# Optimization experiments

Measured on AMD Instinct MI355X. Metric: run time of the kernel, lower is better.

Reference implementation:

```python
import jax, jax.numpy as jnp
import numpy as np

L = 26        # layers (hard-coded NUM_LAYERS)
B, T = 1, 16  # batch, query length
D = 768       # d_model
NH, NG = 8, 2 # heads, query groups
G = NH // NG  # group size
HD = 128      # head_dim
FF = 3072     # ffn hidden
V = 32000     # vocab
SC = 4096     # kv cache length
SOFTCAP = 50.0
EPS = 1e-6


def rms_norm(x, w):
    # zero-centered RMSNorm: x * rsqrt(mean(x^2)+eps) * (1 + w)
    ms = jnp.mean(jnp.square(x), axis=-1, keepdims=True)
    return x * jax.lax.rsqrt(ms + EPS) * (1.0 + w)


def apply_rope(x, cos, sin):
    d = x.shape[-1]
    xl, xr = x[..., : d // 2], x[..., d // 2 :]
    rot = jnp.concatenate([-xr, xl], axis=-1)
    return x * cos + rot * sin


def setup_inputs() -> dict:
    key = jax.random.key(0)
    ks = iter(jax.random.split(key, 40))
    n = lambda shape, s=1.0: jax.random.normal(next(ks), shape, jnp.float32) * s
    u = lambda shape: jax.random.uniform(next(ks), shape, jnp.float32)
    return {
        "embeddings": n((B, T, D)),
        "mask_global": jnp.zeros((B, 1, T, SC + T), jnp.float32),
        "mask_local": jnp.zeros((B, 1, T, SC + T), jnp.float32),
        "pos_emb_cos": u((1, T, 1, HD)),
        "pos_emb_sin": u((1, T, 1, HD)),
        "pos_emb_local_cos": u((1, T, 1, HD)),
        "pos_emb_local_sin": u((1, T, 1, HD)),
        "kv_cache_k": n((L, B, NG, SC, HD)),        # concat on axis 2 (seq)
        "kv_cache_v": n((L, B, NG, HD, SC)),        # concat on axis 3 (seq), V stored transposed
        "pre_attn_norm_w": n((L, D), 0.02),
        "qkv_w": n((L, NG * (G + 2) * HD, D), 0.02),
        "q_norm_w": n((L, HD), 0.02),
        "k_norm_w": n((L, HD), 0.02),
        "out_w": n((L, D, NH * HD), 0.02),
        "post_attn_norm_w": n((L, D), 0.02),
        "pre_ff_norm_w": n((L, D), 0.02),
        "gate_w": n((L, FF, D), 0.02),
        "up_w": n((L, FF, D), 0.02),
        "down_w": n((L, D, FF), 0.02),
        "post_ff_norm_w": n((L, D), 0.02),
        "final_norm_w": n((D,), 0.02),
        "lm_head_w": n((V, D), 0.02),
    }


def reference(embeddings, mask_global, mask_local, pos_emb_cos, pos_emb_sin,
              pos_emb_local_cos, pos_emb_local_sin, kv_cache_k, kv_cache_v,
              pre_attn_norm_w, qkv_w, q_norm_w, k_norm_w, out_w, post_attn_norm_w,
              pre_ff_norm_w, gate_w, up_w, down_w, post_ff_norm_w,
              final_norm_w, lm_head_w):
    is_local = jnp.array([(i + 1) % 6 == 0 for i in range(L)])
    scale = 1.0 / np.sqrt(HD)

    def layer(h, xs):
        pan, qkvw, qnw, knw, ow, postw, pfn, gw, uw, dw, pofn, kc, vc, loc = xs
        cos = jnp.where(loc, pos_emb_local_cos, pos_emb_cos)
        sin = jnp.where(loc, pos_emb_local_sin, pos_emb_sin)
        mask = jnp.where(loc, mask_local, mask_global)

        x = rms_norm(h, pan)
        qkv = jnp.einsum('btd,od->bto', x, qkvw)
        qkv = qkv.reshape(B, T, NG, G + 2, HD).transpose(0, 2, 1, 3, 4)  # [B,NG,T,G+2,HD]
        # faithful to torch: [B,NG,T,G,HD].reshape(B,NH,T,HD) (row-major), then -> [B,T,NH,HD]
        q = qkv[:, :, :, :G, :].reshape(B, NH, T, HD).transpose(0, 2, 1, 3)
        k = qkv[:, :, :, G, :].transpose(0, 2, 1, 3)      # [B,T,NG,HD]
        v = qkv[:, :, :, G + 1, :].transpose(0, 2, 1, 3)  # [B,T,NG,HD]

        q = apply_rope(rms_norm(q, qnw), cos, sin)
        k = apply_rope(rms_norm(k, knw), cos, sin)

        k_new = k.transpose(0, 2, 1, 3)   # [B,NG,T,HD]
        v_new = v.transpose(0, 2, 3, 1)   # [B,NG,HD,T]
        k_full = jnp.concatenate([kc, k_new], axis=2)  # [B,NG,S,HD]
        v_full = jnp.concatenate([vc, v_new], axis=3)  # [B,NG,HD,S]
        k_full = jnp.repeat(k_full, G, axis=1)         # GQA repeat_interleave -> [B,NH,S,HD]
        v_full = jnp.repeat(v_full, G, axis=1)         # [B,NH,HD,S]

        q_a = q.transpose(0, 2, 1, 3)                  # [B,NH,T,HD]
        scores = jnp.einsum('bhtd,bhsd->bhts', q_a, k_full) * scale
        scores = jnp.tanh(scores / SOFTCAP) * SOFTCAP
        probs = jax.nn.softmax(scores + mask, axis=-1)
        attn = jnp.einsum('bhts,bhds->bhtd', probs, v_full)
        attn = attn.transpose(0, 2, 1, 3).reshape(B, T, NH * HD)

        y = jnp.einsum('bto,do->btd', attn, ow)
        h = h + rms_norm(y, postw)

        x2 = rms_norm(h, pfn)
        ff = jnp.einsum('btf,df->btd',
                        jax.nn.gelu(x2 @ gw.T, approximate=True) * (x2 @ uw.T), dw)
        h = h + rms_norm(ff, pofn)
        return h, (k_new, v_new)

    xs = (pre_attn_norm_w, qkv_w, q_norm_w, k_norm_w, out_w, post_attn_norm_w,
          pre_ff_norm_w, gate_w, up_w, down_w, post_ff_norm_w,
          kv_cache_k, kv_cache_v, is_local)
    h, (k_slices, v_slices) = jax.lax.scan(layer, embeddings, xs)
    logits = rms_norm(h, final_norm_w) @ lm_head_w.T
    return logits, k_slices, v_slices
```

## Files before the change

kernel.cpp:

```cpp
#include <hip/hip_runtime.h>
#include <hip/hip_bf16.h>
#include <math.h>

#define NL 26
#define TT 16
#define DD 768
#define HDD 128
#define FFF 3072
#define VV 32000
#define SCCH 4096
#define STOT 4112
#define OQKV 1536
#define EPSF 1e-6f
#define SCALEQ 0.08838834764831845f
#define NCH 65

__device__ __forceinline__ float d4(const float4 a, const float4 b) {
    return fmaf(a.x, b.x, fmaf(a.y, b.y, fmaf(a.z, b.z, a.w * b.w)));
}
__device__ __forceinline__ float4 fma4(float p, const float4 v, float4 a) {
    return make_float4(fmaf(p, v.x, a.x), fmaf(p, v.y, a.y),
                       fmaf(p, v.z, a.z), fmaf(p, v.w, a.w));
}
__device__ __forceinline__ float4 f4add4(float4 a, float4 b, float4 c, float4 d) {
    return make_float4((a.x + b.x) + (c.x + d.x), (a.y + b.y) + (c.y + d.y),
                       (a.z + b.z) + (c.z + d.z), (a.w + b.w) + (c.w + d.w));
}
__device__ __forceinline__ float4 f4res(float4 h, float4 f, float s, float4 w) {
    return make_float4(fmaf(f.x * s, 1.f + w.x, h.x), fmaf(f.y * s, 1.f + w.y, h.y),
                       fmaf(f.z * s, 1.f + w.z, h.z), fmaf(f.w * s, 1.f + w.w, h.w));
}
__device__ __forceinline__ float4 f4nrm(float4 h, float s, float4 w) {
    return make_float4(h.x * s * (1.f + w.x), h.y * s * (1.f + w.y),
                       h.z * s * (1.f + w.z), h.w * s * (1.f + w.w));
}
__device__ __forceinline__ float r16(float v) {
    v += __shfl_xor(v, 1); v += __shfl_xor(v, 2); v += __shfl_xor(v, 4); v += __shfl_xor(v, 8);
    return v;
}
__device__ __forceinline__ float r8(float v) {
    v += __shfl_xor(v, 1); v += __shfl_xor(v, 2); v += __shfl_xor(v, 4);
    return v;
}
__device__ __forceinline__ float rwave(float v) {
    v += __shfl_xor(v, 32); v += __shfl_xor(v, 16); v += __shfl_xor(v, 8);
    v += __shfl_xor(v, 4);  v += __shfl_xor(v, 2);  v += __shfl_xor(v, 1);
    return v;
}

template <int K4>
__device__ __forceinline__ void gemv_row2(const float4* __restrict__ wa,
                                          const float4* __restrict__ wb,
                                          const float* __restrict__ xs, int lane,
                                          float* __restrict__ acca,
                                          float* __restrict__ accb) {
#pragma unroll
    for (int t = 0; t < TT; t++) { acca[t] = 0.f; accb[t] = 0.f; }
    const float4* x4 = reinterpret_cast<const float4*>(xs);
#pragma unroll
    for (int it = 0; it < K4 / 64; ++it) {
        float4 a = wa[it * 64 + lane];
        float4 b = wb[it * 64 + lane];
#pragma unroll
        for (int t = 0; t < TT; t++) {
            float4 x = x4[t * K4 + it * 64 + lane];
            acca[t] = fmaf(a.x, x.x, fmaf(a.y, x.y, fmaf(a.z, x.z, fmaf(a.w, x.w, acca[t]))));
            accb[t] = fmaf(b.x, x.x, fmaf(b.y, x.y, fmaf(b.z, x.z, fmaf(b.w, x.w, accb[t]))));
        }
    }
#pragma unroll
    for (int t = 0; t < TT; t++) { acca[t] = rwave(acca[t]); accb[t] = rwave(accb[t]); }
}

__global__ __launch_bounds__(256) void k_qkv(const int first,
                                             const float* __restrict__ hB,
                                             const float* __restrict__ ff,
                                             const float* __restrict__ emb,
                                             const float* __restrict__ pofn_prev,
                                             const float* __restrict__ pan,
                                             const float* __restrict__ W,
                                             float* __restrict__ qkvo,
                                             float* __restrict__ hA) {
    __shared__ __align__(16) float xs[TT * DD];
    const int tid = threadIdx.x;
    const int row = tid >> 4, c16 = tid & 15;
    float4* xr = reinterpret_cast<float4*>(xs) + row * 192;
    float4* hA4 = reinterpret_cast<float4*>(hA) + row * 192;
    if (first) {
        const float4* e4 = reinterpret_cast<const float4*>(emb) + row * 192;
        float ss = 0.f;
#pragma unroll
        for (int k = 0; k < 12; k++) { int i = c16 + 16 * k; float4 v = e4[i]; xr[i] = v; ss += d4(v, v); }
        ss = r16(ss);
        float inv = rsqrtf(ss * (1.f / 768.f) + EPSF);
        if (blockIdx.x == 0) {
#pragma unroll
            for (int k = 0; k < 12; k++) { int i = c16 + 16 * k; hA4[i] = xr[i]; }
        }
        const float4* p4 = reinterpret_cast<const float4*>(pan);
#pragma unroll
        for (int k = 0; k < 12; k++) { int i = c16 + 16 * k; xr[i] = f4nrm(xr[i], inv, p4[i]); }
    } else {
        const float4* f0 = reinterpret_cast<const float4*>(ff) + row * 192;
        const float4* f1 = f0 + TT * 192;
        const float4* f2 = f1 + TT * 192;
        const float4* f3 = f2 + TT * 192;
        float ss = 0.f;
#pragma unroll
        for (int k = 0; k < 12; k++) {
            int i = c16 + 16 * k;
            float4 v = f4add4(f0[i], f1[i], f2[i], f3[i]);
            xr[i] = v; ss += d4(v, v);
        }
        ss = r16(ss);
        float inv = rsqrtf(ss * (1.f / 768.f) + EPSF);
        const float4* hb4 = reinterpret_cast<const float4*>(hB) + row * 192;
        const float4* po4 = reinterpret_cast<const float4*>(pofn_prev);
        float ss2 = 0.f;
#pragma unroll
        for (int k = 0; k < 12; k++) {
            int i = c16 + 16 * k;
            float4 v = f4res(hb4[i], xr[i], inv, po4[i]);
            xr[i] = v; ss2 += d4(v, v);
            if (blockIdx.x == 0) hA4[i] = v;
        }
        ss2 = r16(ss2);
        float inv2 = rsqrtf(ss2 * (1.f / 768.f) + EPSF);
        const float4* p4 = reinterpret_cast<const float4*>(pan);
#pragma unroll
        for (int k = 0; k < 12; k++) { int i = c16 + 16 * k; xr[i] = f4nrm(xr[i], inv2, p4[i]); }
    }
    __syncthreads();
    const int wv = tid >> 6, lane = tid & 63;
    const int o0 = blockIdx.x * 8 + wv;
    const int o1 = o0 + 4;
    float acca[TT], accb[TT];
    gemv_row2<192>(reinterpret_cast<const float4*>(W + (size_t)o0 * DD),
                   reinterpret_cast<const float4*>(W + (size_t)o1 * DD), xs, lane, acca, accb);
    if (lane < TT) {
        qkvo[lane * OQKV + o0] = acca[lane];
        qkvo[lane * OQKV + o1] = accb[lane];
    }
}

__global__ __launch_bounds__(256) void k_attn(const float* __restrict__ qkv,
                                              const float* __restrict__ kc,
                                              const float* __restrict__ vc,
                                              const float* __restrict__ cosp,
                                              const float* __restrict__ sinp,
                                              const float* __restrict__ mask,
                                              const float* __restrict__ qnw,
                                              const float* __restrict__ knw,
                                              float* __restrict__ part,
                                              float* __restrict__ kout,
                                              float* __restrict__ vout)
{
    __shared__ __align__(16) float kvb[64 * 132];
    __shared__ __align__(16) float pls[16 * 68];
    const int tid = threadIdx.x;
    const int c = blockIdx.x;
    const int ng = blockIdx.y;
    const int rq = blockIdx.z;
    const bool newc = (c == 64);

    {
        int rl = tid >> 4, c16 = tid & 15;
        int r = rq * 16 + rl;
        int tsrc = r >> 2, g = r & 3;
        const float* src = qkv + tsrc * OQKV + ng * 768 + g * 128;
        float ss = 0.f;
#pragma unroll
        for (int j = 0; j < 8; j++) { float v = src[c16 * 8 + j]; ss += v * v; }
        ss = r16(ss);
        float inv = rsqrtf(ss * (1.f / 128.f) + EPSF);
        int pos = r & 15;
        const float* cp = cosp + pos * 128;
        const float* sp = sinp + pos * 128;
#pragma unroll
        for (int j = 0; j < 8; j++) {
            int d = c16 * 8 + j;
            float xn = src[d] * inv * (1.f + qnw[d]);
            float out;
            if (d < 64) { float pr = src[d + 64] * inv * (1.f + qnw[d + 64]); out = xn * cp[d] - pr * sp[d]; }
            else        { float pr = src[d - 64] * inv * (1.f + qnw[d - 64]); out = xn * cp[d] + pr * sp[d]; }
            kvb[rl * 132 + d] = out;
        }
    }
    const int rr = tid >> 4;
    const int half = (tid >> 3) & 1;
    const int dq = tid & 7;
    float4 qreg[4];
    {
        const float4* q4 = reinterpret_cast<const float4*>(kvb + rr * 132);
#pragma unroll
        for (int m = 0; m < 4; m++) qreg[m] = q4[dq + 8 * m];
    }
    __syncthreads();
    if (!newc) {
        int rowk = tid >> 2, q4i = tid & 3;
        const float4* k4 = reinterpret_cast<const float4*>(kc + (size_t)(ng * SCCH + c * 64 + rowk) * 128);
#pragma unroll
        for (int k = 0; k < 8; k++) {
            float4 v = k4[q4i * 8 + k];
            *reinterpret_cast<float4*>(&kvb[rowk * 132 + 4 * (q4i * 8 + k)]) = v;
        }
    } else {
        int t = tid >> 4, c16 = tid & 15;
        const float* src = qkv + t * OQKV + ng * 768 + 4 * 128;
        float ss = 0.f;
#pragma unroll
        for (int j = 0; j < 8; j++) { float v = src[c16 * 8 + j]; ss += v * v; }
        ss = r16(ss);
        float inv = rsqrtf(ss * (1.f / 128.f) + EPSF);
        const float* cp = cosp + t * 128;
        const float* sp = sinp + t * 128;
#pragma unroll
        for (int j = 0; j < 8; j++) {
            int d = c16 * 8 + j;
            float xn = src[d] * inv * (1.f + knw[d]);
            float out;
            if (d < 64) { float pr = src[d + 64] * inv * (1.f + knw[d + 64]); out = xn * cp[d] - pr * sp[d]; }
            else        { float pr = src[d - 64] * inv * (1.f + knw[d - 64]); out = xn * cp[d] + pr * sp[d]; }
            kvb[t * 132 + d] = out;
            if (rq == 0) kout[(ng * TT + t) * 128 + d] = out;
        }
        for (int i = tid; i < 48 * 132; i += 256) kvb[16 * 132 + i] = 0.f;
    }
    __syncthreads();
    const int r = rq * 16 + rr;
    const int pos = r & 15;
    const int cnt_pos = newc ? TT : 64;
    const float* mrow = mask + pos * STOT + c * 64;
    float* prow = pls + rr * 68;
#pragma unroll 4
    for (int jj = 0; jj < 32; jj++) {
        int i = half * 32 + jj;
        const float4* krow = reinterpret_cast<const float4*>(kvb + i * 132);
        float p = d4(qreg[0], krow[dq]) + d4(qreg[1], krow[dq + 8])
                + d4(qreg[2], krow[dq + 16]) + d4(qreg[3], krow[dq + 24]);
        p += __shfl_xor(p, 1); p += __shfl_xor(p, 2); p += __shfl_xor(p, 4);
        if (i < cnt_pos) {
            p *= SCALEQ;
            p = 50.f * tanhf(p * 0.02f);
            p += mrow[i];
        } else {
            p = -1e30f;
        }
        prow[i] = p;
    }
    {
        const float4* prow4 = reinterpret_cast<const float4*>(prow);
        float m = -1e30f;
#pragma unroll 4
        for (int w = 0; w < 16; w++) {
            float4 v = prow4[w];
            m = fmaxf(m, fmaxf(fmaxf(v.x, v.y), fmaxf(v.z, v.w)));
        }
        float lsum = 0.f;
#pragma unroll 4
        for (int w = 0; w < 16; w++) {
            float4 v = prow4[w];
            lsum += (__expf(v.x - m) + __expf(v.y - m)) + (__expf(v.z - m) + __expf(v.w - m));
        }
#pragma unroll 2
        for (int j = 0; j < 4; j++) {
            int i = half * 32 + 8 * j + dq;
            prow[i] = __expf(prow[i] - m);
        }
        if ((tid & 15) == 0) {
            float* pb = part + (size_t)((ng * NCH + c) * 64 + r) * 132;
            pb[128] = m; pb[129] = lsum;
        }
    }
    __syncthreads();
    if (!newc) {
        int d = tid >> 1, hv = tid & 1;
        const float4* v4 = reinterpret_cast<const float4*>(vc + (size_t)(ng * 128 + d) * SCCH + c * 64);
#pragma unroll
        for (int k = 0; k < 8; k++) {
            float4 v = v4[hv * 8 + k];
            int sl = hv * 32 + 4 * k;
            kvb[(sl + 0) * 132 + d] = v.x;
            kvb[(sl + 1) * 132 + d] = v.y;
            kvb[(sl + 2) * 132 + d] = v.z;
            kvb[(sl + 3) * 132 + d] = v.w;
        }
    } else {
        int t = tid >> 4, c16 = tid & 15;
        const float* src = qkv + t * OQKV + ng * 768 + 5 * 128;
#pragma unroll
        for (int j = 0; j < 8; j++) {
            int d = c16 * 8 + j;
            float v = src[d];
            kvb[t * 132 + d] = v;
            if (rq == 0) vout[(ng * 128 + d) * TT + t] = v;
        }
    }
    __syncthreads();
    float4 accv[4];
#pragma unroll
    for (int m2 = 0; m2 < 4; m2++) accv[m2] = make_float4(0.f, 0.f, 0.f, 0.f);
#pragma unroll 4
    for (int jj = 0; jj < 32; jj++) {
        int i = half * 32 + jj;
        float p = prow[i];
        const float4* v4 = reinterpret_cast<const float4*>(kvb + i * 132);
        accv[0] = fma4(p, v4[dq], accv[0]);
        accv[1] = fma4(p, v4[dq + 8], accv[1]);
        accv[2] = fma4(p, v4[dq + 16], accv[2]);
        accv[3] = fma4(p, v4[dq + 24], accv[3]);
    }
#pragma unroll
    for (int m2 = 0; m2 < 4; m2++) {
        accv[m2].x += __shfl_xor(accv[m2].x, 8);
        accv[m2].y += __shfl_xor(accv[m2].y, 8);
        accv[m2].z += __shfl_xor(accv[m2].z, 8);
        accv[m2].w += __shfl_xor(accv[m2].w, 8);
    }
    if (half == 0) {
        float* pb = part + (size_t)((ng * NCH + c) * 64 + r) * 132;
        float4* pb4 = reinterpret_cast<float4*>(pb);
        pb4[dq] = accv[0]; pb4[dq + 8] = accv[1]; pb4[dq + 16] = accv[2]; pb4[dq + 24] = accv[3];
    }
}

__global__ __launch_bounds__(128) void k_combine(const float* __restrict__ part,
                                                 float* __restrict__ attn) {
    __shared__ float marr[NCH], larr[NCH], warr[NCH];
    __shared__ __align__(16) float mrg[4][128];
    int blk = blockIdx.x;
    int ng = blk >> 6, r = blk & 63;
    int tid = threadIdx.x;
    const float* pb = part + (size_t)(ng * NCH * 64 + r) * 132;
    if (tid < NCH) {
        marr[tid] = pb[(size_t)tid * 64 * 132 + 128];
        larr[tid] = pb[(size_t)tid * 64 * 132 + 129];
    }
    __syncthreads();
    float M = -1e30f;
#pragma unroll 4
    for (int cc = 0; cc < NCH; cc++) M = fmaxf(M, marr[cc]);
    if (tid < NCH) warr[tid] = __expf(marr[tid] - M);
    __syncthreads();
    float Lsum = 0.f;
#pragma unroll 4
    for (int cc = 0; cc < NCH; cc++) Lsum = fmaf(larr[cc], warr[cc], Lsum);
    int q = tid >> 5, dd = tid & 31;
    float4 A4 = make_float4(0.f, 0.f, 0.f, 0.f);
    for (int cc = q; cc < NCH; cc += 4) {
        const float4* pa = reinterpret_cast<const float4*>(pb + (size_t)cc * 64 * 132);
        A4 = fma4(warr[cc], pa[dd], A4);
    }
    *reinterpret_cast<float4*>(&mrg[q][dd * 4]) = A4;
    __syncthreads();
    int d = tid;
    float A = (mrg[0][d] + mrg[1][d]) + (mrg[2][d] + mrg[3][d]);
    int h = ng * 4 + (r >> 4), pos = r & 15;
    attn[pos * 1024 + h * 128 + d] = A / Lsum;
}

__global__ __launch_bounds__(256) void k_outproj(const float* __restrict__ W,
                                                 const float* __restrict__ attn,
                                                 float* __restrict__ y) {
    int tid = threadIdx.x;
    int wv = tid >> 6, lane = tid & 63;
    int o0 = blockIdx.x * 8 + wv;
    int o1 = o0 + 4;
    float acca[TT], accb[TT];
    gemv_row2<256>(reinterpret_cast<const float4*>(W + (size_t)o0 * 1024),
                   reinterpret_cast<const float4*>(W + (size_t)o1 * 1024), attn, lane, acca, accb);
    if (lane < TT) {
        y[lane * DD + o0] = acca[lane];
        y[lane * DD + o1] = accb[lane];
    }
}

__global__ __launch_bounds__(256) void k_gateup(const float* __restrict__ hA,
                                                const float* __restrict__ y,
                                                const float* __restrict__ postw,
                                                const float* __restrict__ pfn,
                                                const float* __restrict__ gw,
                                                const float* __restrict__ uw,
                                                float* __restrict__ act,
                                                float* __restrict__ hB) {
    __shared__ __align__(16) float xs[TT * DD];
    int tid = threadIdx.x;
    int row = tid >> 4, c16 = tid & 15;
    float4* xr = reinterpret_cast<float4*>(xs) + row * 192;
    const float4* y4 = reinterpret_cast<const float4*>(y) + row * 192;
    float ss = 0.f;
#pragma unroll
    for (int k = 0; k < 12; k++) { int i = c16 + 16 * k; float4 v = y4[i]; xr[i] = v; ss += d4(v, v); }
    ss = r16(ss);
    float inv = rsqrtf(ss * (1.f / 768.f) + EPSF);
    const float4* ha4 = reinterpret_cast<const float4*>(hA) + row * 192;
    const float4* pw4 = reinterpret_cast<const float4*>(postw);
    float4* hB4 = reinterpret_cast<float4*>(hB) + row * 192;
    float ss2 = 0.f;
#pragma unroll
    for (int k = 0; k < 12; k++) {
        int i = c16 + 16 * k;
        float4 v = f4res(ha4[i], xr[i], inv, pw4[i]);
        xr[i] = v; ss2 += d4(v, v);
        if (blockIdx.x == 0) hB4[i] = v;
    }
    ss2 = r16(ss2);
    float inv2 = rsqrtf(ss2 * (1.f / 768.f) + EPSF);
    const float4* pf4 = reinterpret_cast<const float4*>(pfn);
#pragma unroll
    for (int k = 0; k < 12; k++) { int i = c16 + 16 * k; xr[i] = f4nrm(xr[i], inv2, pf4[i]); }
    __syncthreads();
    int wv = tid >> 6, lane = tid & 63;
    int f0 = blockIdx.x * 8 + wv;
    int f1 = f0 + 4;
    float ag0[TT], ag1[TT], au0[TT], au1[TT];
    gemv_row2<192>(reinterpret_cast<const float4*>(gw + (size_t)f0 * DD),
                   reinterpret_cast<const float4*>(gw + (size_t)f1 * DD), xs, lane, ag0, ag1);
    gemv_row2<192>(reinterpret_cast<const float4*>(uw + (size_t)f0 * DD),
                   reinterpret_cast<const float4*>(uw + (size_t)f1 * DD), xs, lane, au0, au1);
    if (lane < TT) {
        {
            float g = ag0[lane], u = au0[lane];
            float inner = 0.7978845608028654f * fmaf(0.044715f * g, g * g, g);
            float gel = 0.5f * g * (1.f + tanhf(inner));
            act[lane * FFF + f0] = gel * u;
        }
        {
            float g = ag1[lane], u = au1[lane];
            float inner = 0.7978845608028654f * fmaf(0.044715f * g, g * g, g);
            float gel = 0.5f * g * (1.f + tanhf(inner));
            act[lane * FFF + f1] = gel * u;
        }
    }
}

__global__ __launch_bounds__(256) void k_down(const float* __restrict__ W,
                                              const float* __restrict__ act,
                                              float* __restrict__ ffp) {
    __shared__ __align__(16) float xs[TT * DD];
    int tid = threadIdx.x;
    int fq = blockIdx.x & 3, dc = blockIdx.x >> 2;
    {
        const float4* a4 = reinterpret_cast<const float4*>(act);
        float4* s4 = reinterpret_cast<float4*>(xs);
#pragma unroll
        for (int k = 0; k < 12; k++) {
            int i = tid + 256 * k;
            int t = i / 192, cq = i - t * 192;
            s4[i] = a4[t * 768 + fq * 192 + cq];
        }
    }
    __syncthreads();
    int wv = tid >> 6, lane = tid & 63;
    int o0 = dc * 8 + wv;
    int o1 = o0 + 4;
    float acca[TT], accb[TT];
    gemv_row2<192>(reinterpret_cast<const float4*>(W + (size_t)o0 * FFF + fq * 768),
                   reinterpret_cast<const float4*>(W + (size_t)o1 * FFF + fq * 768), xs, lane, acca, accb);
    if (lane < TT) {
        ffp[(fq * TT + lane) * DD + o0] = acca[lane];
        ffp[(fq * TT + lane) * DD + o1] = accb[lane];
    }
}

__global__ __launch_bounds__(256) void k_lmfused(const float* __restrict__ hB,
                                                 const float* __restrict__ ff,
                                                 const float* __restrict__ pofn25,
                                                 const float* __restrict__ fnw,
                                                 const float* __restrict__ W,
                                                 float* __restrict__ logits) {
    __shared__ __align__(16) float xs[TT * DD];
    int tid = threadIdx.x;
    int row = tid >> 4, c16 = tid & 15;
    float4* xr = reinterpret_cast<float4*>(xs) + row * 192;
    const float4* f0 = reinterpret_cast<const float4*>(ff) + row * 192;
    const float4* f1 = f0 + TT * 192;
    const float4* f2 = f1 + TT * 192;
    const float4* f3 = f2 + TT * 192;
    float ss = 0.f;
#pragma unroll
    for (int k = 0; k < 12; k++) {
        int i = c16 + 16 * k;
        float4 v = f4add4(f0[i], f1[i], f2[i], f3[i]);
        xr[i] = v; ss += d4(v, v);
    }
    ss = r16(ss);
    float inv = rsqrtf(ss * (1.f / 768.f) + EPSF);
    const float4* hb4 = reinterpret_cast<const float4*>(hB) + row * 192;
    const float4* po4 = reinterpret_cast<const float4*>(pofn25);
    float ss2 = 0.f;
#pragma unroll
    for (int k = 0; k < 12; k++) {
        int i = c16 + 16 * k;
        float4 v = f4res(hb4[i], xr[i], inv, po4[i]);
        xr[i] = v; ss2 += d4(v, v);
    }
    ss2 = r16(ss2);
    float inv2 = rsqrtf(ss2 * (1.f / 768.f) + EPSF);
    const float4* fn4 = reinterpret_cast<const float4*>(fnw);
#pragma unroll
    for (int k = 0; k < 12; k++) { int i = c16 + 16 * k; xr[i] = f4nrm(xr[i], inv2, fn4[i]); }
    __syncthreads();
    int wv = tid >> 6, lane = tid & 63;
#pragma unroll
    for (int rr = 0; rr < 8; ++rr) {
        int o0 = blockIdx.x * 64 + rr * 8 + wv;
        int o1 = o0 + 4;
        float acca[TT], accb[TT];
        gemv_row2<192>(reinterpret_cast<const float4*>(W + (size_t)o0 * DD),
                       reinterpret_cast<const float4*>(W + (size_t)o1 * DD), xs, lane, acca, accb);
        if (lane < TT) {
            logits[lane * VV + o0] = acca[lane];
            logits[lane * VV + o1] = accb[lane];
        }
    }
}

extern "C" void kernel_launch(void* const* d_in, const int* in_sizes, int n_in,
                              void* d_out, int out_size, void* d_ws, size_t ws_size,
                              hipStream_t stream) {
    const float* emb   = (const float*)d_in[0];
    const float* maskg = (const float*)d_in[1];
    const float* maskl = (const float*)d_in[2];
    const float* cosg  = (const float*)d_in[3];
    const float* sing  = (const float*)d_in[4];
    const float* cosl  = (const float*)d_in[5];
    const float* sinl  = (const float*)d_in[6];
    const float* kck   = (const float*)d_in[7];
    const float* kcv   = (const float*)d_in[8];
    const float* pan   = (const float*)d_in[9];
    const float* qkvw  = (const float*)d_in[10];
    const float* qnw   = (const float*)d_in[11];
    const float* knw   = (const float*)d_in[12];
    const float* outw  = (const float*)d_in[13];
    const float* postw = (const float*)d_in[14];
    const float* pfnw  = (const float*)d_in[15];
    const float* gw    = (const float*)d_in[16];
    const float* uw    = (const float*)d_in[17];
    const float* dw    = (const float*)d_in[18];
    const float* pofn  = (const float*)d_in[19];
    const float* fnw   = (const float*)d_in[20];
    const float* lmw   = (const float*)d_in[21];

    float* ws   = (float*)d_ws;
    float* hA   = ws;
    float* hB   = hA + 12288;
    float* qkvb = hB + 12288;
    float* attnb = qkvb + 24576;
    float* yb   = attnb + 16384;
    float* act  = yb + 12288;
    float* ffp  = act + 49152;
    float* part = ffp + 49152;

    float* outp = (float*)d_out;
    float* outK = outp + 512000;
    float* outV = outK + 106496;

    for (int l = 0; l < NL; l++) {
        int loc = ((l + 1) % 6) == 0;
        const float* cosp = loc ? cosl : cosg;
        const float* sinp = loc ? sinl : sing;
        const float* maskp = loc ? maskl : maskg;
        k_qkv<<<192, 256, 0, stream>>>(l == 0 ? 1 : 0, hB, ffp, emb,
                                       l ? (pofn + (size_t)(l - 1) * DD) : pofn,
                                       pan + (size_t)l * DD,
                                       qkvw + (size_t)l * OQKV * DD, qkvb, hA);
        k_attn<<<dim3(NCH, 2, 4), 256, 0, stream>>>(qkvb,
                                                    kck + (size_t)l * 2 * SCCH * HDD,
                                                    kcv + (size_t)l * 2 * HDD * SCCH,
                                                    cosp, sinp, maskp,
                                                    qnw + (size_t)l * HDD, knw + (size_t)l * HDD,
                                                    part,
                                                    outK + (size_t)l * 2 * TT * HDD,
                                                    outV + (size_t)l * 2 * HDD * TT);
        k_combine<<<128, 128, 0, stream>>>(part, attnb);
        k_outproj<<<96, 256, 0, stream>>>(outw + (size_t)l * DD * 1024, attnb, yb);
        k_gateup<<<384, 256, 0, stream>>>(hA, yb, postw + (size_t)l * DD, pfnw + (size_t)l * DD,
                                          gw + (size_t)l * FFF * DD, uw + (size_t)l * FFF * DD,
                                          act, hB);
        k_down<<<384, 256, 0, stream>>>(dw + (size_t)l * DD * FFF, act, ffp);
    }
    k_lmfused<<<500, 256, 0, stream>>>(hB, ffp, pofn + (size_t)25 * DD, fnw, lmw, outp);
}
```

Measured before the change: 2.868 ms.

## Replace split-softmax combine with fixed-max exp and atomic accumulation

After: 2.925 ms. Within noise of the previous version (+2.0%).

```diff
diff --git a/kernel.cpp b/kernel.cpp
--- a/kernel.cpp
+++ b/kernel.cpp
@@ -14,6 +14,7 @@
 #define EPSF 1e-6f
 #define SCALEQ 0.08838834764831845f
 #define NCH 65
+#define M0 12.0f
 
 __device__ __forceinline__ float d4(const float4 a, const float4 b) {
     return fmaf(a.x, b.x, fmaf(a.y, b.y, fmaf(a.z, b.z, a.w * b.w)));
@@ -36,16 +37,17 @@
 }
 __device__ __forceinline__ float r16(float v) {
     v += __shfl_xor(v, 1); v += __shfl_xor(v, 2); v += __shfl_xor(v, 4); v += __shfl_xor(v, 8);
-    return v;
-}
-__device__ __forceinline__ float r8(float v) {
-    v += __shfl_xor(v, 1); v += __shfl_xor(v, 2); v += __shfl_xor(v, 4);
     return v;
 }
 __device__ __forceinline__ float rwave(float v) {
     v += __shfl_xor(v, 32); v += __shfl_xor(v, 16); v += __shfl_xor(v, 8);
     v += __shfl_xor(v, 4);  v += __shfl_xor(v, 2);  v += __shfl_xor(v, 1);
     return v;
+}
+__device__ __forceinline__ float ftanh(float x) {
+    float t = __expf(-2.f * fabsf(x));
+    float th = (1.f - t) / (1.f + t);
+    return copysignf(th, x);
 }
 
 template <int K4>
@@ -70,6 +72,39 @@
     }
 #pragma unroll
     for (int t = 0; t < TT; t++) { acca[t] = rwave(acca[t]); accb[t] = rwave(accb[t]); }
+}
+
+template <int K4>
+__device__ __forceinline__ void gemv_row4(const float4* __restrict__ wa,
+                                          const float4* __restrict__ wb,
+                                          const float4* __restrict__ wc,
+                                          const float4* __restrict__ wd,
+                                          const float* __restrict__ xs, int lane,
+                                          float* __restrict__ acca, float* __restrict__ accb,
+                                          float* __restrict__ accc, float* __restrict__ accd) {
+#pragma unroll
+    for (int t = 0; t < TT; t++) { acca[t] = 0.f; accb[t] = 0.f; accc[t] = 0.f; accd[t] = 0.f; }
+    const float4* x4 = reinterpret_cast<const float4*>(xs);
+#pragma unroll
+    for (int it = 0; it < K4 / 64; ++it) {
+        float4 a = wa[it * 64 + lane];
+        float4 b = wb[it * 64 + lane];
+        float4 c = wc[it * 64 + lane];
+        float4 d = wd[it * 64 + lane];
+#pragma unroll
+        for (int t = 0; t < TT; t++) {
+            float4 x = x4[t * K4 + it * 64 + lane];
+            acca[t] = fmaf(a.x, x.x, fmaf(a.y, x.y, fmaf(a.z, x.z, fmaf(a.w, x.w, acca[t]))));
+            accb[t] = fmaf(b.x, x.x, fmaf(b.y, x.y, fmaf(b.z, x.z, fmaf(b.w, x.w, accb[t]))));
+            accc[t] = fmaf(c.x, x.x, fmaf(c.y, x.y, fmaf(c.z, x.z, fmaf(c.w, x.w, accc[t]))));
+            accd[t] = fmaf(d.x, x.x, fmaf(d.y, x.y, fmaf(d.z, x.z, fmaf(d.w, x.w, accd[t]))));
+        }
+    }
+#pragma unroll
+    for (int t = 0; t < TT; t++) {
+        acca[t] = rwave(acca[t]); accb[t] = rwave(accb[t]);
+        accc[t] = rwave(accc[t]); accd[t] = rwave(accd[t]);
+    }
 }
 
 __global__ __launch_bounds__(256) void k_qkv(const int first,
@@ -80,10 +115,12 @@
                                              const float* __restrict__ pan,
                                              const float* __restrict__ W,
                                              float* __restrict__ qkvo,
-                                             float* __restrict__ hA) {
+                                             float* __restrict__ hA,
+                                             float* __restrict__ attnz) {
     __shared__ __align__(16) float xs[TT * DD];
     const int tid = threadIdx.x;
     const int row = tid >> 4, c16 = tid & 15;
+    for (int i = blockIdx.x * 256 + tid; i < 16512; i += 192 * 256) attnz[i] = 0.f;
     float4* xr = reinterpret_cast<float4*>(xs) + row * 192;
     float4* hA4 = reinterpret_cast<float4*>(hA) + row * 192;
     if (first) {
@@ -151,7 +188,8 @@
                                               const float* __restrict__ mask,
                                               const float* __restrict__ qnw,
                                               const float* __restrict__ knw,
-                                              float* __restrict__ part,
+                                              float* __restrict__ attnb_u,
+                                              float* __restrict__ lsumb,
                                               float* __restrict__ kout,
                                               float* __restrict__ vout)
 {
@@ -232,6 +270,7 @@
     const int cnt_pos = newc ? TT : 64;
     const float* mrow = mask + pos * STOT + c * 64;
     float* prow = pls + rr * 68;
+    float ls = 0.f;
 #pragma unroll 4
     for (int jj = 0; jj < 32; jj++) {
         int i = half * 32 + jj;
@@ -239,38 +278,21 @@
         float p = d4(qreg[0], krow[dq]) + d4(qreg[1], krow[dq + 8])
                 + d4(qreg[2], krow[dq + 16]) + d4(qreg[3], krow[dq + 24]);
         p += __shfl_xor(p, 1); p += __shfl_xor(p, 2); p += __shfl_xor(p, 4);
+        float pe;
         if (i < cnt_pos) {
             p *= SCALEQ;
-            p = 50.f * tanhf(p * 0.02f);
-            p += mrow[i];
+            p = 50.f * ftanh(p * 0.02f);
+            pe = __expf(p + mrow[i] - M0);
         } else {
-            p = -1e30f;
-        }
-        prow[i] = p;
-    }
-    {
-        const float4* prow4 = reinterpret_cast<const float4*>(prow);
-        float m = -1e30f;
-#pragma unroll 4
-        for (int w = 0; w < 16; w++) {
-            float4 v = prow4[w];
-            m = fmaxf(m, fmaxf(fmaxf(v.x, v.y), fmaxf(v.z, v.w)));
-        }
-        float lsum = 0.f;
-#pragma unroll 4
-        for (int w = 0; w < 16; w++) {
-            float4 v = prow4[w];
-            lsum += (__expf(v.x - m) + __expf(v.y - m)) + (__expf(v.z - m) + __expf(v.w - m));
-        }
-#pragma unroll 2
-        for (int j = 0; j < 4; j++) {
-            int i = half * 32 + 8 * j + dq;
-            prow[i] = __expf(prow[i] - m);
-        }
-        if ((tid & 15) == 0) {
-            float* pb = part + (size_t)((ng * NCH + c) * 64 + r) * 132;
-            pb[128] = m; pb[129] = lsum;
-        }
+            pe = 0.f;
+        }
+        prow[i] = pe;
+        ls += pe;
+    }
+    ls += __shfl_xor(ls, 8);
+    if ((tid & 15) == 0) {
+        int h = ng * 4 + (r >> 4);
+        atomicAdd(&lsumb[pos * 8 + h], ls);
     }
     __syncthreads();
     if (!newc) {
@@ -318,57 +340,52 @@
         accv[m2].w += __shfl_xor(accv[m2].w, 8);
     }
     if (half == 0) {
-        float* pb = part + (size_t)((ng * NCH + c) * 64 + r) * 132;
-        float4* pb4 = reinterpret_cast<float4*>(pb);
-        pb4[dq] = accv[0]; pb4[dq + 8] = accv[1]; pb4[dq + 16] = accv[2]; pb4[dq + 24] = accv[3];
-    }
-}
-
-__global__ __launch_bounds__(128) void k_combine(const float* __restrict__ part,
-                                                 float* __restrict__ attn) {
-    __shared__ float marr[NCH], larr[NCH], warr[NCH];
-    __shared__ __align__(16) float mrg[4][128];
-    int blk = blockIdx.x;
-    int ng = blk >> 6, r = blk & 63;
+        int h = ng * 4 + (r >> 4);
+        float* ab = attnb_u + pos * 1024 + h * 128;
+#pragma unroll
+        for (int m2 = 0; m2 < 4; m2++) {
+            int d0 = dq * 4 + 32 * m2;
+            atomicAdd(&ab[d0 + 0], accv[m2].x);
+            atomicAdd(&ab[d0 + 1], accv[m2].y);
+            atomicAdd(&ab[d0 + 2], accv[m2].z);
+            atomicAdd(&ab[d0 + 3], accv[m2].w);
+        }
+    }
+}
+
+__global__ __launch_bounds__(256) void k_outproj(const float* __restrict__ W,
+                                                 const float* __restrict__ attnb_u,
+                                                 const float* __restrict__ lsumb,
+                                                 float* __restrict__ y) {
+    __shared__ float invl[128];
     int tid = threadIdx.x;
-    const float* pb = part + (size_t)(ng * NCH * 64 + r) * 132;
-    if (tid < NCH) {
-        marr[tid] = pb[(size_t)tid * 64 * 132 + 128];
-        larr[tid] = pb[(size_t)tid * 64 * 132 + 129];
-    }
-    __syncthreads();
-    float M = -1e30f;
-#pragma unroll 4
-    for (int cc = 0; cc < NCH; cc++) M = fmaxf(M, marr[cc]);
-    if (tid < NCH) warr[tid] = __expf(marr[tid] - M);
-    __syncthreads();
-    float Lsum = 0.f;
-#pragma unroll 4
-    for (int cc = 0; cc < NCH; cc++) Lsum = fmaf(larr[cc], warr[cc], Lsum);
-    int q = tid >> 5, dd = tid & 31;
-    float4 A4 = make_float4(0.f, 0.f, 0.f, 0.f);
-    for (int cc = q; cc < NCH; cc += 4) {
-        const float4* pa = reinterpret_cast<const float4*>(pb + (size_t)cc * 64 * 132);
-        A4 = fma4(warr[cc], pa[dd], A4);
-    }
-    *reinterpret_cast<float4*>(&mrg[q][dd * 4]) = A4;
-    __syncthreads();
-    int d = tid;
-    float A = (mrg[0][d] + mrg[1][d]) + (mrg[2][d] + mrg[3][d]);
-    int h = ng * 4 + (r >> 4), pos = r & 15;
-    attn[pos * 1024 + h * 128 + d] = A / Lsum;
-}
-
-__global__ __launch_bounds__(256) void k_outproj(const float* __restrict__ W,
-                                                 const float* __restrict__ attn,
-                                                 float* __restrict__ y) {
-    int tid = threadIdx.x;
+    if (tid < 128) invl[tid] = 1.f / lsumb[tid];
+    __syncthreads();
     int wv = tid >> 6, lane = tid & 63;
     int o0 = blockIdx.x * 8 + wv;
     int o1 = o0 + 4;
+    const float4* wa = reinterpret_cast<const float4*>(W + (size_t)o0 * 1024);
+    const float4* wb = reinterpret_cast<const float4*>(W + (size_t)o1 * 1024);
+    const float4* a4 = reinterpret_cast<const float4*>(attnb_u);
     float acca[TT], accb[TT];
-    gemv_row2<256>(reinterpret_cast<const float4*>(W + (size_t)o0 * 1024),
-                   reinterpret_cast<const float4*>(W + (size_t)o1 * 1024), attn, lane, acca, accb);
+#pragma unroll
+    for (int t = 0; t < TT; t++) { acca[t] = 0.f; accb[t] = 0.f; }
+#pragma unroll
+    for (int it = 0; it < 4; ++it) {
+        float4 a = wa[it * 64 + lane];
+        float4 b = wb[it * 64 + lane];
+        int hh = (it * 64 + lane) >> 5;
+#pragma unroll
+        for (int t = 0; t < TT; t++) {
+            float4 x = a4[t * 256 + it * 64 + lane];
+            float s = invl[t * 8 + hh];
+            x.x *= s; x.y *= s; x.z *= s; x.w *= s;
+            acca[t] = fmaf(a.x, x.x, fmaf(a.y, x.y, fmaf(a.z, x.z, fmaf(a.w, x.w, acca[t]))));
+            accb[t] = fmaf(b.x, x.x, fmaf(b.y, x.y, fmaf(b.z, x.z, fmaf(b.w, x.w, accb[t]))));
+        }
+    }
+#pragma unroll
+    for (int t = 0; t < TT; t++) { acca[t] = rwave(acca[t]); accb[t] = rwave(accb[t]); }
     if (lane < TT) {
         y[lane * DD + o0] = acca[lane];
         y[lane * DD + o1] = accb[lane];
@@ -414,21 +431,22 @@
     int f0 = blockIdx.x * 8 + wv;
     int f1 = f0 + 4;
     float ag0[TT], ag1[TT], au0[TT], au1[TT];
-    gemv_row2<192>(reinterpret_cast<const float4*>(gw + (size_t)f0 * DD),
-                   reinterpret_cast<const float4*>(gw + (size_t)f1 * DD), xs, lane, ag0, ag1);
-    gemv_row2<192>(reinterpret_cast<const float4*>(uw + (size_t)f0 * DD),
-                   reinterpret_cast<const float4*>(uw + (size_t)f1 * DD), xs, lane, au0, au1);
+    gemv_row4<192>(reinterpret_cast<const float4*>(gw + (size_t)f0 * DD),
+                   reinterpret_cast<const float4*>(gw + (size_t)f1 * DD),
+                   reinterpret_cast<const float4*>(uw + (size_t)f0 * DD),
+                   reinterpret_cast<const float4*>(uw + (size_t)f1 * DD),
+                   xs, lane, ag0, ag1, au0, au1);
     if (lane < TT) {
         {
             float g = ag0[lane], u = au0[lane];
             float inner = 0.7978845608028654f * fmaf(0.044715f * g, g * g, g);
-            float gel = 0.5f * g * (1.f + tanhf(inner));
+            float gel = 0.5f * g * (1.f + ftanh(inner));
             act[lane * FFF + f0] = gel * u;
         }
         {
             float g = ag1[lane], u = au1[lane];
             float inner = 0.7978845608028654f * fmaf(0.044715f * g, g * g, g);
-            float gel = 0.5f * g * (1.f + tanhf(inner));
+            float gel = 0.5f * g * (1.f + ftanh(inner));
             act[lane * FFF + f1] = gel * u;
         }
     }
@@ -547,10 +565,10 @@
     float* hB   = hA + 12288;
     float* qkvb = hB + 12288;
     float* attnb = qkvb + 24576;
-    float* yb   = attnb + 16384;
+    float* lsumb = attnb + 16384;
+    float* yb   = lsumb + 128;
     float* act  = yb + 12288;
     float* ffp  = act + 49152;
-    float* part = ffp + 49152;
 
     float* outp = (float*)d_out;
     float* outK = outp + 512000;
@@ -564,17 +582,16 @@
         k_qkv<<<192, 256, 0, stream>>>(l == 0 ? 1 : 0, hB, ffp, emb,
                                        l ? (pofn + (size_t)(l - 1) * DD) : pofn,
                                        pan + (size_t)l * DD,
-                                       qkvw + (size_t)l * OQKV * DD, qkvb, hA);
+                                       qkvw + (size_t)l * OQKV * DD, qkvb, hA, attnb);
         k_attn<<<dim3(NCH, 2, 4), 256, 0, stream>>>(qkvb,
                                                     kck + (size_t)l * 2 * SCCH * HDD,
                                                     kcv + (size_t)l * 2 * HDD * SCCH,
                                                     cosp, sinp, maskp,
                                                     qnw + (size_t)l * HDD, knw + (size_t)l * HDD,
-                                                    part,
+                                                    attnb, lsumb,
                                                     outK + (size_t)l * 2 * TT * HDD,
                                                     outV + (size_t)l * 2 * HDD * TT);
-        k_combine<<<128, 128, 0, stream>>>(part, attnb);
-        k_outproj<<<96, 256, 0, stream>>>(outw + (size_t)l * DD * 1024, attnb, yb);
+        k_outproj<<<96, 256, 0, stream>>>(outw + (size_t)l * DD * 1024, attnb, lsumb, yb);
         k_gateup<<<384, 256, 0, stream>>>(hA, yb, postw + (size_t)l * DD, pfnw + (size_t)l * DD,
                                           gw + (size_t)l * FFF * DD, uw + (size_t)l * FFF * DD,
                                           act, hB);
```
